# Kernel optimization log

Measured on AMD Instinct MI355X. Metric: run time of the kernel, lower is better.

The kernel has to match this reference:

```python
import jax, jax.numpy as jnp
from jax import lax
import numpy as np

N = 65536
D = 512
NUM_STEPS = 10
TIME_INTERVAL = 1.0


def setup_inputs() -> dict:
    key = jax.random.key(0)
    ks = jax.random.split(key, 8)
    s1 = 1.0 / np.sqrt(D + 1)
    s2 = 1.0 / np.sqrt(D)
    sg = 1.0 / np.sqrt(2 * D)
    return {
        "current_node_features": jax.random.normal(ks[0], (N, D), jnp.float32),
        "previous_hidden_state": jax.random.normal(ks[1], (N, D), jnp.float32),
        # torch nn.Linear layout: weight [out, in], bias [out]
        "W1": jax.random.uniform(ks[2], (D, D + 1), jnp.float32, -s1, s1),
        "b1": jax.random.uniform(ks[3], (D,), jnp.float32, -s1, s1),
        "W2": jax.random.uniform(ks[4], (D, D), jnp.float32, -s2, s2),
        "b2": jax.random.uniform(ks[5], (D,), jnp.float32, -s2, s2),
        "Wg": jax.random.uniform(ks[6], (D, 2 * D), jnp.float32, -sg, sg),
        "bg": jax.random.uniform(ks[7], (D,), jnp.float32, -sg, sg),
    }


def reference(current_node_features, previous_hidden_state, W1, b1, W2, b2, Wg, bg):
    x = current_node_features
    dt = jnp.asarray(TIME_INTERVAL / NUM_STEPS, x.dtype)
    n = x.shape[0]

    def euler_step(h, t):
        # concat time feature: [N, D+1]
        time_col = jnp.full((n, 1), t, h.dtype)
        z = jnp.concatenate([h, time_col], axis=-1)
        deriv = jnp.tanh(jnp.tanh(z @ W1.T + b1) @ W2.T + b2)
        return h + dt * deriv, None

    ts = jnp.arange(NUM_STEPS, dtype=x.dtype) * dt  # t_i = start + i*dt
    evolved, _ = lax.scan(euler_step, previous_hidden_state, ts)

    combined = jnp.concatenate([x, evolved], axis=-1)  # [N, 2D]
    gate = jax.nn.sigmoid(combined @ Wg.T + bg)
    updated = gate * evolved + (1.0 - gate) * x
    return updated, updated
```

## Files before the change

### kernel.cpp

```cpp
#include <hip/hip_runtime.h>

#define N_ROWS 65536
#define DIM    512
#define NSTEP  10

typedef float  f32x16 __attribute__((ext_vector_type(16)));
typedef float  f32x4  __attribute__((ext_vector_type(4)));
typedef short  s16x8  __attribute__((ext_vector_type(8)));
typedef __bf16 bf16x8 __attribute__((ext_vector_type(8)));
typedef unsigned int u32x2 __attribute__((ext_vector_type(2)));
typedef unsigned int u32x4 __attribute__((ext_vector_type(4)));

__device__ __forceinline__ unsigned f2bf(float f) {
  unsigned u = __float_as_uint(f);
  return (u + 0x7fffu + ((u >> 16) & 1u)) >> 16;
}
__device__ __forceinline__ unsigned pack2bf_rn(float a, float b) {
  unsigned ua = __float_as_uint(a) + 0x8000u;
  unsigned ub = __float_as_uint(b) + 0x8000u;
  return __builtin_amdgcn_perm(ub, ua, 0x07060302u);
}
#define LOG2E_X2 2.885390081777927f
#define LOG2E    1.442695040888963f
__device__ __forceinline__ float ftanh(float x) {
  float t = __builtin_amdgcn_exp2f(x * LOG2E_X2);
  float r = __builtin_amdgcn_rcpf(1.0f + t);
  return __builtin_fmaf(-2.0f, r, 1.0f);
}
__device__ __forceinline__ float fsigm(float x) {
  float t = __builtin_amdgcn_exp2f(-x * LOG2E);
  return __builtin_amdgcn_rcpf(1.0f + t);
}
__device__ __forceinline__ void mfma(f32x16& c, s16x8 a, s16x8 b) {
  c = __builtin_amdgcn_mfma_f32_32x32x16_bf16(
        __builtin_bit_cast(bf16x8, a), __builtin_bit_cast(bf16x8, b), c, 0, 0, 0);
}

__global__ void pack_frags_kernel(const float* __restrict__ src, int row_stride,
                                  int col_off, unsigned short* __restrict__ dst) {
  const int idx = blockIdx.x * 256 + threadIdx.x;
  const int l    = idx & 63;
  const int frag = idx >> 6;
  const int otg  = frag >> 5;
  const int ks   = frag & 31;
  const int o = otg * 32 + (l & 31);
  const int k = ks * 16 + (l >> 5) * 8;
  const float* p = src + (size_t)o * row_stride + col_off + k;
  s16x8 v;
#pragma unroll
  for (int i = 0; i < 8; ++i) v[i] = (short)f2bf(p[i]);
  *reinterpret_cast<s16x8*>(dst + (size_t)idx * 8) = v;
}

__global__ void c1_kernel(const float* __restrict__ W1, const float* __restrict__ b1,
                          float* __restrict__ c1) {
  const int o = threadIdx.x;
  const float wt = W1[(size_t)o * 513 + 512];
  const float bb = b1[o];
  for (int s = 0; s < NSTEP; ++s)
    c1[s * DIM + o] = bb + ((float)s * 0.1f) * wt;
}

__global__ __launch_bounds__(512, 2)
void ode_fused(const float* __restrict__ x, const float* __restrict__ h0,
               const float* __restrict__ b2, const float* __restrict__ bg,
               const s16x8* __restrict__ w1f, const s16x8* __restrict__ w2f,
               const s16x8* __restrict__ wgaf, const s16x8* __restrict__ wgbf,
               const float* __restrict__ c1, float* __restrict__ out)
{
  __shared__ char ldsA[64 * 1024];
  __shared__ char ldsB[64 * 1024];

  const int tid = threadIdx.x;
  const int w   = tid >> 6;
  const int l   = tid & 63;
  const int lm  = l & 31;
  const int h5  = l >> 5;
  const int m0  = blockIdx.x << 6;
  const int ow  = w << 6;
  const unsigned lbyte = (unsigned)l << 4;

  {
#pragma unroll
    for (int q = 0; q < 8; ++q) {
      const int f  = (w << 3) | q;
      const int ks = f >> 1;
      const int mt = f & 1;
      const float* src = h0 + (size_t)(m0 + (mt << 5) + lm) * DIM + (ks << 4) + (h5 << 3);
      f32x4 v0 = *reinterpret_cast<const f32x4*>(src);
      f32x4 v1 = *reinterpret_cast<const f32x4*>(src + 4);
      u32x4 pk;
      pk[0] = pack2bf_rn(v0[0], v0[1]); pk[1] = pack2bf_rn(v0[2], v0[3]);
      pk[2] = pack2bf_rn(v1[0], v1[1]); pk[3] = pack2bf_rn(v1[2], v1[3]);
      *reinterpret_cast<u32x4*>(ldsA + (f << 10) + lbyte) = pk;
    }
  }

  f32x16 hst[2][2];
#pragma unroll
  for (int ot = 0; ot < 2; ++ot)
#pragma unroll
    for (int mt = 0; mt < 2; ++mt) {
      const float* hr = h0 + (size_t)(m0 + (mt << 5) + lm) * DIM;
#pragma unroll
      for (int g = 0; g < 4; ++g) {
        const int oc = ow + (ot << 5) + (g << 3) + (h5 << 2);
        f32x4 v = *reinterpret_cast<const f32x4*>(hr + oc);
#pragma unroll
        for (int j = 0; j < 4; ++j) hst[ot][mt][(g << 2) + j] = v[j];
      }
    }

  f32x16 acc[2][2];

  auto mm_lds = [&](const s16x8* __restrict__ A, const char* __restrict__ buf) {
    const s16x8* A0 = A + (w << 12);
    const s16x8* A1 = A0 + 2048;
#pragma unroll 4
    for (int ks = 0; ks < 32; ++ks) {
      s16x8 a0 = A0[(ks << 6) + l];
      s16x8 a1 = A1[(ks << 6) + l];
      s16x8 b0 = *reinterpret_cast<const s16x8*>(buf + (ks << 11) + lbyte);
      s16x8 b1 = *reinterpret_cast<const s16x8*>(buf + (ks << 11) + 1024 + lbyte);
      mfma(acc[0][0], a0, b0);
      mfma(acc[0][1], a0, b1);
      mfma(acc[1][0], a1, b0);
      mfma(acc[1][1], a1, b1);
    }
  };

  auto acc_init = [&](const float* __restrict__ vec) {
#pragma unroll
    for (int ot = 0; ot < 2; ++ot)
#pragma unroll
      for (int g = 0; g < 4; ++g) {
        const int oc = ow + (ot << 5) + (g << 3) + (h5 << 2);
        f32x4 v = *reinterpret_cast<const f32x4*>(vec + oc);
#pragma unroll
        for (int mt = 0; mt < 2; ++mt)
#pragma unroll
          for (int j = 0; j < 4; ++j) acc[ot][mt][(g << 2) + j] = v[j];
      }
  };

  auto tile_write = [&](const f32x16 src[2][2], char* __restrict__ buf) {
    const unsigned base = ((unsigned)w << 13) + ((unsigned)lm << 4) + ((unsigned)h5 << 3);
#pragma unroll
    for (int ot = 0; ot < 2; ++ot)
#pragma unroll
      for (int mt = 0; mt < 2; ++mt)
#pragma unroll
        for (int g = 0; g < 4; ++g) {
          u32x2 pk;
          pk[0] = pack2bf_rn(src[ot][mt][(g << 2) + 0], src[ot][mt][(g << 2) + 1]);
          pk[1] = pack2bf_rn(src[ot][mt][(g << 2) + 2], src[ot][mt][(g << 2) + 3]);
          *reinterpret_cast<u32x2*>(buf + base + (ot << 12) + ((g >> 1) << 11)
                                    + (mt << 10) + ((g & 1) << 9)) = pk;
        }
  };

  __syncthreads();

#pragma unroll 1
  for (int s = 0; s < NSTEP; ++s) {
    acc_init(c1 + s * DIM);
    mm_lds(w1f, ldsA);
#pragma unroll
    for (int ot = 0; ot < 2; ++ot)
#pragma unroll
      for (int mt = 0; mt < 2; ++mt)
#pragma unroll
        for (int i = 0; i < 16; ++i) acc[ot][mt][i] = ftanh(acc[ot][mt][i]);
    tile_write(acc, ldsB);
    __syncthreads();
    acc_init(b2);
    mm_lds(w2f, ldsB);
#pragma unroll
    for (int ot = 0; ot < 2; ++ot)
#pragma unroll
      for (int mt = 0; mt < 2; ++mt)
#pragma unroll
        for (int i = 0; i < 16; ++i) {
          float t = __builtin_amdgcn_exp2f(acc[ot][mt][i] * LOG2E_X2);
          float r = __builtin_amdgcn_rcpf(1.0f + t);
          hst[ot][mt][i] = __builtin_fmaf(-0.2f, r, hst[ot][mt][i] + 0.1f);
        }
    tile_write(hst, ldsA);
    __syncthreads();
  }

  acc_init(bg);
  mm_lds(wgbf, ldsA);
  {
    const s16x8* A0 = wgaf + (w << 12);
    const s16x8* A1 = A0 + 2048;
    const float* xr0 = x + (size_t)(m0 + lm) * DIM + (h5 << 3);
    const float* xr1 = xr0 + (size_t)32 * DIM;
#pragma unroll 2
    for (int ks = 0; ks < 32; ++ks) {
      s16x8 a0 = A0[(ks << 6) + l];
      s16x8 a1 = A1[(ks << 6) + l];
      const int kc = ks << 4;
      f32x4 u0 = *reinterpret_cast<const f32x4*>(xr0 + kc);
      f32x4 u1 = *reinterpret_cast<const f32x4*>(xr0 + kc + 4);
      u32x4 pb;
      pb[0] = pack2bf_rn(u0[0], u0[1]); pb[1] = pack2bf_rn(u0[2], u0[3]);
      pb[2] = pack2bf_rn(u1[0], u1[1]); pb[3] = pack2bf_rn(u1[2], u1[3]);
      s16x8 b0 = __builtin_bit_cast(s16x8, pb);
      f32x4 w0 = *reinterpret_cast<const f32x4*>(xr1 + kc);
      f32x4 w1 = *reinterpret_cast<const f32x4*>(xr1 + kc + 4);
      u32x4 qb;
      qb[0] = pack2bf_rn(w0[0], w0[1]); qb[1] = pack2bf_rn(w0[2], w0[3]);
      qb[2] = pack2bf_rn(w1[0], w1[1]); qb[3] = pack2bf_rn(w1[2], w1[3]);
      s16x8 b1 = __builtin_bit_cast(s16x8, qb);
      mfma(acc[0][0], a0, b0);
      mfma(acc[0][1], a0, b1);
      mfma(acc[1][0], a1, b0);
      mfma(acc[1][1], a1, b1);
    }
  }

  float* out1 = out + (size_t)N_ROWS * DIM;
#pragma unroll
  for (int mt = 0; mt < 2; ++mt) {
    const int m = m0 + (mt << 5) + lm;
    const float* xr = x + (size_t)m * DIM;
    float* o0p = out  + (size_t)m * DIM;
    float* o1p = out1 + (size_t)m * DIM;
#pragma unroll
    for (int ot = 0; ot < 2; ++ot)
#pragma unroll
      for (int g = 0; g < 4; ++g) {
        const int oc = ow + (ot << 5) + (g << 3) + (h5 << 2);
        f32x4 xv = *reinterpret_cast<const f32x4*>(xr + oc);
        f32x4 r;
#pragma unroll
        for (int j = 0; j < 4; ++j) {
          const float gt = fsigm(acc[ot][mt][(g << 2) + j]);
          const float ev = hst[ot][mt][(g << 2) + j];
          r[j] = gt * ev + (1.0f - gt) * xv[j];
        }
        *reinterpret_cast<f32x4*>(o0p + oc) = r;
        *reinterpret_cast<f32x4*>(o1p + oc) = r;
      }
  }
}

extern "C" void kernel_launch(void* const* d_in, const int* in_sizes, int n_in,
                              void* d_out, int out_size, void* d_ws, size_t ws_size,
                              hipStream_t stream) {
  const float* x  = (const float*)d_in[0];
  const float* h0 = (const float*)d_in[1];
  const float* W1 = (const float*)d_in[2];
  const float* b1 = (const float*)d_in[3];
  const float* W2 = (const float*)d_in[4];
  const float* b2 = (const float*)d_in[5];
  const float* Wg = (const float*)d_in[6];
  const float* bg = (const float*)d_in[7];

  char* ws = (char*)d_ws;
  const size_t FRAG_BYTES = (size_t)512 * 512 * 2;
  unsigned short* w1f  = (unsigned short*)(ws + 0 * FRAG_BYTES);
  unsigned short* w2f  = (unsigned short*)(ws + 1 * FRAG_BYTES);
  unsigned short* wgaf = (unsigned short*)(ws + 2 * FRAG_BYTES);
  unsigned short* wgbf = (unsigned short*)(ws + 3 * FRAG_BYTES);
  float*          c1   = (float*)(ws + 4 * FRAG_BYTES);

  pack_frags_kernel<<<128, 256, 0, stream>>>(W1, 513, 0,   w1f);
  pack_frags_kernel<<<128, 256, 0, stream>>>(W2, 512, 0,   w2f);
  pack_frags_kernel<<<128, 256, 0, stream>>>(Wg, 1024, 0,  wgaf);
  pack_frags_kernel<<<128, 256, 0, stream>>>(Wg, 1024, 512, wgbf);
  c1_kernel<<<1, 512, 0, stream>>>(W1, b1, c1);

  ode_fused<<<N_ROWS / 64, 512, 0, stream>>>(x, h0, b2, bg,
                                             (const s16x8*)w1f, (const s16x8*)w2f,
                                             (const s16x8*)wgaf, (const s16x8*)wgbf,
                                             c1, (float*)d_out);
}
```

Measured before the change: 1.002 ms.

## Halve rows per block to cut LDS and raise occupancy

Each workgroup now processes 32 rows instead of 64. This halves the LDS buffers and accumulator registers, and the launch bound is raised to 4 blocks. The aim is more resident waves to hide memory and MFMA latency. In exchange, each weight fragment loaded from global memory feeds only one MFMA instead of two, which doubles weight traffic from L2.

```diff
diff --git a/kernel.cpp b/kernel.cpp
--- a/kernel.cpp
+++ b/kernel.cpp
@@ -61,57 +61,54 @@
     c1[s * DIM + o] = bb + ((float)s * 0.1f) * wt;
 }
 
-__global__ __launch_bounds__(512, 2)
+__global__ __launch_bounds__(512, 4)
 void ode_fused(const float* __restrict__ x, const float* __restrict__ h0,
                const float* __restrict__ b2, const float* __restrict__ bg,
                const s16x8* __restrict__ w1f, const s16x8* __restrict__ w2f,
                const s16x8* __restrict__ wgaf, const s16x8* __restrict__ wgbf,
                const float* __restrict__ c1, float* __restrict__ out)
 {
-  __shared__ char ldsA[64 * 1024];
-  __shared__ char ldsB[64 * 1024];
+  __shared__ char ldsA[32 * 1024];
+  __shared__ char ldsB[32 * 1024];
 
   const int tid = threadIdx.x;
   const int w   = tid >> 6;
   const int l   = tid & 63;
   const int lm  = l & 31;
   const int h5  = l >> 5;
-  const int m0  = blockIdx.x << 6;
+  const int m0  = blockIdx.x << 5;
   const int ow  = w << 6;
   const unsigned lbyte = (unsigned)l << 4;
 
   {
 #pragma unroll
-    for (int q = 0; q < 8; ++q) {
-      const int f  = (w << 3) | q;
-      const int ks = f >> 1;
-      const int mt = f & 1;
-      const float* src = h0 + (size_t)(m0 + (mt << 5) + lm) * DIM + (ks << 4) + (h5 << 3);
+    for (int q = 0; q < 4; ++q) {
+      const int ks = (w << 2) | q;
+      const float* src = h0 + (size_t)(m0 + lm) * DIM + (ks << 4) + (h5 << 3);
       f32x4 v0 = *reinterpret_cast<const f32x4*>(src);
       f32x4 v1 = *reinterpret_cast<const f32x4*>(src + 4);
       u32x4 pk;
       pk[0] = pack2bf_rn(v0[0], v0[1]); pk[1] = pack2bf_rn(v0[2], v0[3]);
       pk[2] = pack2bf_rn(v1[0], v1[1]); pk[3] = pack2bf_rn(v1[2], v1[3]);
-      *reinterpret_cast<u32x4*>(ldsA + (f << 10) + lbyte) = pk;
+      *reinterpret_cast<u32x4*>(ldsA + (ks << 10) + lbyte) = pk;
     }
   }
 
-  f32x16 hst[2][2];
-#pragma unroll
-  for (int ot = 0; ot < 2; ++ot)
-#pragma unroll
-    for (int mt = 0; mt < 2; ++mt) {
-      const float* hr = h0 + (size_t)(m0 + (mt << 5) + lm) * DIM;
+  f32x16 hst[2];
+  {
+    const float* hr = h0 + (size_t)(m0 + lm) * DIM;
+#pragma unroll
+    for (int ot = 0; ot < 2; ++ot)
 #pragma unroll
       for (int g = 0; g < 4; ++g) {
         const int oc = ow + (ot << 5) + (g << 3) + (h5 << 2);
         f32x4 v = *reinterpret_cast<const f32x4*>(hr + oc);
 #pragma unroll
-        for (int j = 0; j < 4; ++j) hst[ot][mt][(g << 2) + j] = v[j];
-      }
-    }
-
-  f32x16 acc[2][2];
+        for (int j = 0; j < 4; ++j) hst[ot][(g << 2) + j] = v[j];
+      }
+  }
+
+  f32x16 acc[2];
 
   auto mm_lds = [&](const s16x8* __restrict__ A, const char* __restrict__ buf) {
     const s16x8* A0 = A + (w << 12);
@@ -120,12 +117,9 @@
     for (int ks = 0; ks < 32; ++ks) {
       s16x8 a0 = A0[(ks << 6) + l];
       s16x8 a1 = A1[(ks << 6) + l];
-      s16x8 b0 = *reinterpret_cast<const s16x8*>(buf + (ks << 11) + lbyte);
-      s16x8 b1 = *reinterpret_cast<const s16x8*>(buf + (ks << 11) + 1024 + lbyte);
-      mfma(acc[0][0], a0, b0);
-      mfma(acc[0][1], a0, b1);
-      mfma(acc[1][0], a1, b0);
-      mfma(acc[1][1], a1, b1);
+      s16x8 b = *reinterpret_cast<const s16x8*>(buf + (ks << 10) + lbyte);
+      mfma(acc[0], a0, b);
+      mfma(acc[1], a1, b);
     }
   };
 
@@ -137,26 +131,22 @@
         const int oc = ow + (ot << 5) + (g << 3) + (h5 << 2);
         f32x4 v = *reinterpret_cast<const f32x4*>(vec + oc);
 #pragma unroll
-        for (int mt = 0; mt < 2; ++mt)
-#pragma unroll
-          for (int j = 0; j < 4; ++j) acc[ot][mt][(g << 2) + j] = v[j];
+        for (int j = 0; j < 4; ++j) acc[ot][(g << 2) + j] = v[j];
       }
   };
 
-  auto tile_write = [&](const f32x16 src[2][2], char* __restrict__ buf) {
-    const unsigned base = ((unsigned)w << 13) + ((unsigned)lm << 4) + ((unsigned)h5 << 3);
-#pragma unroll
-    for (int ot = 0; ot < 2; ++ot)
-#pragma unroll
-      for (int mt = 0; mt < 2; ++mt)
-#pragma unroll
-        for (int g = 0; g < 4; ++g) {
-          u32x2 pk;
-          pk[0] = pack2bf_rn(src[ot][mt][(g << 2) + 0], src[ot][mt][(g << 2) + 1]);
-          pk[1] = pack2bf_rn(src[ot][mt][(g << 2) + 2], src[ot][mt][(g << 2) + 3]);
-          *reinterpret_cast<u32x2*>(buf + base + (ot << 12) + ((g >> 1) << 11)
-                                    + (mt << 10) + ((g & 1) << 9)) = pk;
-        }
+  const unsigned twbase = ((unsigned)w << 12) + ((unsigned)lm << 4) + ((unsigned)h5 << 3);
+  auto tile_write = [&](const f32x16 src[2], char* __restrict__ buf) {
+#pragma unroll
+    for (int ot = 0; ot < 2; ++ot)
+#pragma unroll
+      for (int g = 0; g < 4; ++g) {
+        u32x2 pk;
+        pk[0] = pack2bf_rn(src[ot][(g << 2) + 0], src[ot][(g << 2) + 1]);
+        pk[1] = pack2bf_rn(src[ot][(g << 2) + 2], src[ot][(g << 2) + 3]);
+        *reinterpret_cast<u32x2*>(buf + twbase + (ot << 11) + ((g >> 1) << 10)
+                                  + ((g & 1) << 9)) = pk;
+      }
   };
 
   __syncthreads();
@@ -168,9 +158,7 @@
 #pragma unroll
     for (int ot = 0; ot < 2; ++ot)
 #pragma unroll
-      for (int mt = 0; mt < 2; ++mt)
-#pragma unroll
-        for (int i = 0; i < 16; ++i) acc[ot][mt][i] = ftanh(acc[ot][mt][i]);
+      for (int i = 0; i < 16; ++i) acc[ot][i] = ftanh(acc[ot][i]);
     tile_write(acc, ldsB);
     __syncthreads();
     acc_init(b2);
@@ -178,13 +166,11 @@
 #pragma unroll
     for (int ot = 0; ot < 2; ++ot)
 #pragma unroll
-      for (int mt = 0; mt < 2; ++mt)
-#pragma unroll
-        for (int i = 0; i < 16; ++i) {
-          float t = __builtin_amdgcn_exp2f(acc[ot][mt][i] * LOG2E_X2);
-          float r = __builtin_amdgcn_rcpf(1.0f + t);
-          hst[ot][mt][i] = __builtin_fmaf(-0.2f, r, hst[ot][mt][i] + 0.1f);
-        }
+      for (int i = 0; i < 16; ++i) {
+        float t = __builtin_amdgcn_exp2f(acc[ot][i] * LOG2E_X2);
+        float r = __builtin_amdgcn_rcpf(1.0f + t);
+        hst[ot][i] = __builtin_fmaf(-0.2f, r, hst[ot][i] + 0.1f);
+      }
     tile_write(hst, ldsA);
     __syncthreads();
   }
@@ -194,36 +180,26 @@
   {
     const s16x8* A0 = wgaf + (w << 12);
     const s16x8* A1 = A0 + 2048;
-    const float* xr0 = x + (size_t)(m0 + lm) * DIM + (h5 << 3);
-    const float* xr1 = xr0 + (size_t)32 * DIM;
-#pragma unroll 2
+    const float* xr = x + (size_t)(m0 + lm) * DIM + (h5 << 3);
+#pragma unroll 4
     for (int ks = 0; ks < 32; ++ks) {
       s16x8 a0 = A0[(ks << 6) + l];
       s16x8 a1 = A1[(ks << 6) + l];
       const int kc = ks << 4;
-      f32x4 u0 = *reinterpret_cast<const f32x4*>(xr0 + kc);
-      f32x4 u1 = *reinterpret_cast<const f32x4*>(xr0 + kc + 4);
+      f32x4 u0 = *reinterpret_cast<const f32x4*>(xr + kc);
+      f32x4 u1 = *reinterpret_cast<const f32x4*>(xr + kc + 4);
       u32x4 pb;
       pb[0] = pack2bf_rn(u0[0], u0[1]); pb[1] = pack2bf_rn(u0[2], u0[3]);
       pb[2] = pack2bf_rn(u1[0], u1[1]); pb[3] = pack2bf_rn(u1[2], u1[3]);
-      s16x8 b0 = __builtin_bit_cast(s16x8, pb);
-      f32x4 w0 = *reinterpret_cast<const f32x4*>(xr1 + kc);
-      f32x4 w1 = *reinterpret_cast<const f32x4*>(xr1 + kc + 4);
-      u32x4 qb;
-      qb[0] = pack2bf_rn(w0[0], w0[1]); qb[1] = pack2bf_rn(w0[2], w0[3]);
-      qb[2] = pack2bf_rn(w1[0], w1[1]); qb[3] = pack2bf_rn(w1[2], w1[3]);
-      s16x8 b1 = __builtin_bit_cast(s16x8, qb);
-      mfma(acc[0][0], a0, b0);
-      mfma(acc[0][1], a0, b1);
-      mfma(acc[1][0], a1, b0);
-      mfma(acc[1][1], a1, b1);
+      s16x8 b = __builtin_bit_cast(s16x8, pb);
+      mfma(acc[0], a0, b);
+      mfma(acc[1], a1, b);
     }
   }
 
   float* out1 = out + (size_t)N_ROWS * DIM;
-#pragma unroll
-  for (int mt = 0; mt < 2; ++mt) {
-    const int m = m0 + (mt << 5) + lm;
+  {
+    const int m = m0 + lm;
     const float* xr = x + (size_t)m * DIM;
     float* o0p = out  + (size_t)m * DIM;
     float* o1p = out1 + (size_t)m * DIM;
@@ -236,8 +212,8 @@
         f32x4 r;
 #pragma unroll
         for (int j = 0; j < 4; ++j) {
-          const float gt = fsigm(acc[ot][mt][(g << 2) + j]);
-          const float ev = hst[ot][mt][(g << 2) + j];
+          const float gt = fsigm(acc[ot][(g << 2) + j]);
+          const float ev = hst[ot][(g << 2) + j];
           r[j] = gt * ev + (1.0f - gt) * xv[j];
         }
         *reinterpret_cast<f32x4*>(o0p + oc) = r;
@@ -272,7 +248,7 @@
   pack_frags_kernel<<<128, 256, 0, stream>>>(Wg, 1024, 512, wgbf);
   c1_kernel<<<1, 512, 0, stream>>>(W1, b1, c1);
 
-  ode_fused<<<N_ROWS / 64, 512, 0, stream>>>(x, h0, b2, bg,
+  ode_fused<<<N_ROWS / 32, 512, 0, stream>>>(x, h0, b2, bg,
                                              (const s16x8*)w1f, (const s16x8*)w2f,
                                              (const s16x8*)wgaf, (const s16x8*)wgbf,
                                              c1, (float*)d_out);
```

Result: slower. 1.143 ms (+14.1%).
